# Kernel tuning notes

Hardware: AMD Instinct MI355X
Metric: run time of the kernel (lower is better)

Reference implementation:

```python
import jax, jax.numpy as jnp
import numpy as np
from jax import lax

T, B, IN, H = 26246, 128, 6, 1  # seq_len, batch, input_size, hidden_size(=output_size)

def setup_inputs() -> dict:
    key = jax.random.key(0)
    ks = jax.random.split(key, 7)
    return {
        "x": jax.random.normal(ks[0], (T, B, IN), dtype=jnp.float32),
        "W_ih": jax.random.normal(ks[1], (H, IN), dtype=jnp.float32) * 0.3,
        "W_hh": jax.random.normal(ks[2], (H, H), dtype=jnp.float32) * 0.3,
        "b_ih": jax.random.normal(ks[3], (H,), dtype=jnp.float32) * 0.1,
        "b_hh": jax.random.normal(ks[4], (H,), dtype=jnp.float32) * 0.1,
        "fc_w": jax.random.normal(ks[5], (H, H), dtype=jnp.float32),
        "fc_b": jax.random.normal(ks[6], (H,), dtype=jnp.float32) * 0.1,
    }

def reference(x, W_ih, W_hh, b_ih, b_hh, fc_w, fc_b):
    # Vanilla tanh RNN (nn.RNN, batch_first=False): h_t = tanh(x_t W_ih^T + b_ih + h_{t-1} W_hh^T + b_hh)
    # Precompute the input projection for all timesteps in one GEMM: [T,B,H]
    xp = jnp.einsum('tbi,hi->tbh', x, W_ih) + b_ih + b_hh

    def step(h, xt):  # h: [B,H], xt: [B,H]
        h_new = jnp.tanh(xt + h @ W_hh.T)
        return h_new, h_new

    h0 = jnp.zeros((B, H), dtype=x.dtype)
    _, hs = lax.scan(step, h0, xp)      # hs: [T,B,H] — full output sequence
    # Trailing Linear applied per timestep
    out = hs @ fc_w.T + fc_b            # [T,B,H]
    return out
```

## Files before the change

kernel.cpp:

```cpp
#include <hip/hip_runtime.h>
#include <math.h>

#define T_LEN 26246
#define B_SZ  128
#define SCALE 2.88539008177792681472f

#define CHUNK 104
#define UNR   8
#define NCH   ((T_LEN + CHUNK - 1) / CHUNK)

__global__ __launch_bounds__(128) void rnn_scan_fused(
    const float* __restrict__ x, const float* __restrict__ W_ih,
    const float* __restrict__ W_hh, const float* __restrict__ b_ih,
    const float* __restrict__ b_hh, const float* __restrict__ fc_w,
    const float* __restrict__ fc_b, float* __restrict__ out) {
  const int b  = threadIdx.x;
  const int c  = blockIdx.x;
  const int t0 = c * CHUNK;

  const float w  = W_hh[0];
  const float w2 = SCALE * w;
  const float s0 = SCALE * W_ih[0], s1 = SCALE * W_ih[1], s2 = SCALE * W_ih[2],
              s3 = SCALE * W_ih[3], s4 = SCALE * W_ih[4], s5 = SCALE * W_ih[5];
  const float sb = SCALE * (b_ih[0] + b_hh[0]);
  const float fw = fc_w[0], fb = fc_b[0];

  int warm = 16;
  {
    float aw = fabsf(w);
    if (aw > 0.56f) {
      float l = logf(fminf(aw, 0.999f));
      warm = (int)ceilf(-9.2103404f / l);
      warm = (warm + UNR - 1) & ~(UNR - 1);
      if (warm > 2048) warm = 2048;
    }
  }
  int tw = t0 - warm;
  if (tw < 0) tw = 0;
  const int tlim = t0 + CHUNK;

  float h = 0.0f;
  float2 buf[UNR][3], nbuf[UNR][3];

  #pragma unroll
  for (int j = 0; j < UNR; ++j) {
    int t = tw + j; t = (t < T_LEN) ? t : (T_LEN - 1);
    const float2* p = (const float2*)(x + ((size_t)t * B_SZ + b) * 6);
    buf[j][0] = p[0]; buf[j][1] = p[1]; buf[j][2] = p[2];
  }

  for (int tb = tw; tb < tlim; tb += UNR) {
    #pragma unroll
    for (int j = 0; j < UNR; ++j) {
      int t = tb + UNR + j; t = (t < T_LEN) ? t : (T_LEN - 1);
      const float2* p = (const float2*)(x + ((size_t)t * B_SZ + b) * 6);
      nbuf[j][0] = p[0]; nbuf[j][1] = p[1]; nbuf[j][2] = p[2];
    }
    #pragma unroll
    for (int j = 0; j < UNR; ++j) {
      float a = fmaf(buf[j][0].x, s0, sb);
      a = fmaf(buf[j][0].y, s1, a);
      a = fmaf(buf[j][1].x, s2, a);
      a = fmaf(buf[j][1].y, s3, a);
      a = fmaf(buf[j][2].x, s4, a);
      a = fmaf(buf[j][2].y, s5, a);
      float g = fmaf(h, w2, a);
      float u = __builtin_amdgcn_exp2f(g);
      float r = __builtin_amdgcn_rcpf(u + 1.0f);
      h = fmaf(-2.0f, r, 1.0f);
      const int t = tb + j;
      if (t >= t0 && t < T_LEN) out[(size_t)t * B_SZ + b] = fmaf(h, fw, fb);
    }
    #pragma unroll
    for (int j = 0; j < UNR; ++j) {
      buf[j][0] = nbuf[j][0]; buf[j][1] = nbuf[j][1]; buf[j][2] = nbuf[j][2];
    }
  }
}

extern "C" void kernel_launch(void* const* d_in, const int* in_sizes, int n_in,
                              void* d_out, int out_size, void* d_ws, size_t ws_size,
                              hipStream_t stream) {
  const float* x    = (const float*)d_in[0];
  const float* W_ih = (const float*)d_in[1];
  const float* W_hh = (const float*)d_in[2];
  const float* b_ih = (const float*)d_in[3];
  const float* b_hh = (const float*)d_in[4];
  const float* fc_w = (const float*)d_in[5];
  const float* fc_b = (const float*)d_in[6];
  float* out = (float*)d_out;

  rnn_scan_fused<<<NCH, 128, 0, stream>>>(x, W_ih, W_hh, b_ih, b_hh,
                                          fc_w, fc_b, out);
}
```

Before: 23.94 us.

## Process two batch rows per lane with float4 loads and triple-buffered prefetch

```diff
diff --git a/kernel.cpp b/kernel.cpp
--- a/kernel.cpp
+++ b/kernel.cpp
@@ -6,17 +6,17 @@
 #define SCALE 2.88539008177792681472f
 
 #define CHUNK 104
-#define UNR   8
+#define GS    4
 #define NCH   ((T_LEN + CHUNK - 1) / CHUNK)
+#define TOTAL_F4 ((size_t)T_LEN * 192)
 
-__global__ __launch_bounds__(128) void rnn_scan_fused(
+__global__ __launch_bounds__(64) void rnn_scan_fused(
     const float* __restrict__ x, const float* __restrict__ W_ih,
     const float* __restrict__ W_hh, const float* __restrict__ b_ih,
     const float* __restrict__ b_hh, const float* __restrict__ fc_w,
     const float* __restrict__ fc_b, float* __restrict__ out) {
-  const int b  = threadIdx.x;
-  const int c  = blockIdx.x;
-  const int t0 = c * CHUNK;
+  const int lane = threadIdx.x;
+  const int t0   = blockIdx.x * CHUNK;
 
   const float w  = W_hh[0];
   const float w2 = SCALE * w;
@@ -31,51 +31,75 @@
     if (aw > 0.56f) {
       float l = logf(fminf(aw, 0.999f));
       warm = (int)ceilf(-9.2103404f / l);
-      warm = (warm + UNR - 1) & ~(UNR - 1);
+      warm = (warm + GS - 1) & ~(GS - 1);
       if (warm > 2048) warm = 2048;
     }
   }
   int tw = t0 - warm;
   if (tw < 0) tw = 0;
-  const int tlim = t0 + CHUNK;
+  const int tlim = (t0 + CHUNK < T_LEN) ? (t0 + CHUNK) : T_LEN;
+  const int gtot = (tlim - tw + GS - 1) / GS;
 
-  float h = 0.0f;
-  float2 buf[UNR][3], nbuf[UNR][3];
+  const float4* x4 = (const float4*)x;
 
-  #pragma unroll
-  for (int j = 0; j < UNR; ++j) {
-    int t = tw + j; t = (t < T_LEN) ? t : (T_LEN - 1);
-    const float2* p = (const float2*)(x + ((size_t)t * B_SZ + b) * 6);
-    buf[j][0] = p[0]; buf[j][1] = p[1]; buf[j][2] = p[2];
+  float4 bufA[GS][3], bufB[GS][3], bufC[GS][3];
+  float h0 = 0.0f, h1 = 0.0f;
+
+  #define LOADG(buf, g)                                                   \
+    {                                                                     \
+      _Pragma("unroll")                                                   \
+      for (int e = 0; e < GS; ++e) {                                      \
+        int t = tw + GS * (g) + e;                                        \
+        t = (t < T_LEN) ? t : (T_LEN - 1);                                \
+        size_t base = (size_t)t * 192 + 3 * (size_t)lane;                 \
+        buf[e][0] = x4[base]; buf[e][1] = x4[base + 1];                   \
+        buf[e][2] = x4[base + 2];                                         \
+      }                                                                   \
+    }
+
+  #define STEPG(buf, g)                                                   \
+    {                                                                     \
+      _Pragma("unroll")                                                   \
+      for (int e = 0; e < GS; ++e) {                                      \
+        const int t = tw + GS * (g) + e;                                  \
+        float a0 = fmaf(buf[e][0].x, s0, sb);                             \
+        a0 = fmaf(buf[e][0].y, s1, a0);                                   \
+        a0 = fmaf(buf[e][0].z, s2, a0);                                   \
+        a0 = fmaf(buf[e][0].w, s3, a0);                                   \
+        a0 = fmaf(buf[e][1].x, s4, a0);                                   \
+        a0 = fmaf(buf[e][1].y, s5, a0);                                   \
+        float a1 = fmaf(buf[e][1].z, s0, sb);                             \
+        a1 = fmaf(buf[e][1].w, s1, a1);                                   \
+        a1 = fmaf(buf[e][2].x, s2, a1);                                   \
+        a1 = fmaf(buf[e][2].y, s3, a1);                                   \
+        a1 = fmaf(buf[e][2].z, s4, a1);                                   \
+        a1 = fmaf(buf[e][2].w, s5, a1);                                   \
+        float g0 = fmaf(h0, w2, a0);                                      \
+        float g1 = fmaf(h1, w2, a1);                                      \
+        float u0 = __builtin_amdgcn_exp2f(g0);                            \
+        float u1 = __builtin_amdgcn_exp2f(g1);                            \
+        float r0 = __builtin_amdgcn_rcpf(u0 + 1.0f);                      \
+        float r1 = __builtin_amdgcn_rcpf(u1 + 1.0f);                      \
+        h0 = fmaf(-2.0f, r0, 1.0f);                                       \
+        h1 = fmaf(-2.0f, r1, 1.0f);                                       \
+        if (t >= t0 && t < tlim) {                                        \
+          float2* op = (float2*)(out + (size_t)t * B_SZ + 2 * lane);      \
+          *op = make_float2(fmaf(h0, fw, fb), fmaf(h1, fw, fb));          \
+        }                                                                 \
+      }                                                                   \
+    }
+
+  LOADG(bufA, 0);
+  LOADG(bufB, 1);
+  LOADG(bufC, 2);
+
+  for (int g = 0; g < gtot; g += 3) {
+    STEPG(bufA, g);     LOADG(bufA, g + 3);
+    STEPG(bufB, g + 1); LOADG(bufB, g + 4);
+    STEPG(bufC, g + 2); LOADG(bufC, g + 5);
   }
-
-  for (int tb = tw; tb < tlim; tb += UNR) {
-    #pragma unroll
-    for (int j = 0; j < UNR; ++j) {
-      int t = tb + UNR + j; t = (t < T_LEN) ? t : (T_LEN - 1);
-      const float2* p = (const float2*)(x + ((size_t)t * B_SZ + b) * 6);
-      nbuf[j][0] = p[0]; nbuf[j][1] = p[1]; nbuf[j][2] = p[2];
-    }
-    #pragma unroll
-    for (int j = 0; j < UNR; ++j) {
-      float a = fmaf(buf[j][0].x, s0, sb);
-      a = fmaf(buf[j][0].y, s1, a);
-      a = fmaf(buf[j][1].x, s2, a);
-      a = fmaf(buf[j][1].y, s3, a);
-      a = fmaf(buf[j][2].x, s4, a);
-      a = fmaf(buf[j][2].y, s5, a);
-      float g = fmaf(h, w2, a);
-      float u = __builtin_amdgcn_exp2f(g);
-      float r = __builtin_amdgcn_rcpf(u + 1.0f);
-      h = fmaf(-2.0f, r, 1.0f);
-      const int t = tb + j;
-      if (t >= t0 && t < T_LEN) out[(size_t)t * B_SZ + b] = fmaf(h, fw, fb);
-    }
-    #pragma unroll
-    for (int j = 0; j < UNR; ++j) {
-      buf[j][0] = nbuf[j][0]; buf[j][1] = nbuf[j][1]; buf[j][2] = nbuf[j][2];
-    }
-  }
+  #undef LOADG
+  #undef STEPG
 }
 
 extern "C" void kernel_launch(void* const* d_in, const int* in_sizes, int n_in,
@@ -90,6 +114,6 @@
   const float* fc_b = (const float*)d_in[6];
   float* out = (float*)d_out;
 
-  rnn_scan_fused<<<NCH, 128, 0, stream>>>(x, W_ih, W_hh, b_ih, b_hh,
-                                          fc_w, fc_b, out);
+  rnn_scan_fused<<<NCH, 64, 0, stream>>>(x, W_ih, W_hh, b_ih, b_hh,
+                                         fc_w, fc_b, out);
 }
```

Result: slower. 28.34 us (+18.4%).
